# Performance work log

Hardware: AMD Instinct MI355X
Metric: run time of the kernel (lower is better)

## Reference

```python
import jax, jax.numpy as jnp
import numpy as np


def _mlp2(x, W1, b1, W2, b2):
    # two-layer MLP with ReLU hidden activation
    h = jax.nn.relu(jnp.einsum('...i,ij->...j', x, W1) + b1)
    return jnp.einsum('...i,ij->...j', h, W2) + b2


def setup_inputs() -> dict:
    key = jax.random.key(0)
    ks = jax.random.split(key, 8)
    B, N, D = 8, 256, 64
    positions = jax.random.normal(ks[0], (B, N, 3), dtype=jnp.float32)
    values = jax.random.normal(ks[1], (B, N, D), dtype=jnp.float32)
    # value_net: 2 -> D -> D ; score_net: D -> D -> 1 (He-style init)
    Wv1 = jax.random.normal(ks[2], (2, D), dtype=jnp.float32) * np.sqrt(2.0 / 2)
    bv1 = jnp.zeros((D,), dtype=jnp.float32)
    Wv2 = jax.random.normal(ks[3], (D, D), dtype=jnp.float32) * np.sqrt(2.0 / D)
    bv2 = jnp.zeros((D,), dtype=jnp.float32)
    Ws1 = jax.random.normal(ks[4], (D, D), dtype=jnp.float32) * np.sqrt(2.0 / D)
    bs1 = jnp.zeros((D,), dtype=jnp.float32)
    Ws2 = jax.random.normal(ks[5], (D, 1), dtype=jnp.float32) * np.sqrt(2.0 / D)
    bs2 = jnp.zeros((1,), dtype=jnp.float32)
    return dict(positions=positions, values=values, Wv1=Wv1, bv1=bv1, Wv2=Wv2,
                bv2=bv2, Ws1=Ws1, bs1=bs1, Ws2=Ws2, bs2=bs2)


def reference(positions, values, Wv1, bv1, Wv2, bv2, Ws1, bs1, Ws2, bs2):
    # rank-2 geometric algebra attention, reduce=True, merge_fun=join_fun='mean'
    B, N, _ = positions.shape
    r_i = positions[:, :, None, :]            # [B, N, 1, 3]
    r_j = positions[:, None, :, :]            # [B, 1, N, 3]
    # geometric product of two vectors -> scalar (dot) + bivector (wedge)
    dot = jnp.sum(r_i * r_j, axis=-1)         # [B, N, N] scalar part
    wedge = jnp.cross(r_i, r_j)               # [B, N, N, 3] bivector components
    biv_norm = jnp.sqrt(jnp.sum(wedge * wedge, axis=-1) + 1e-20)
    invariants = jnp.stack([dot, biv_norm], axis=-1)             # [B, N, N, 2]
    # merge_fun='mean' over the pair of node values
    merged = 0.5 * (values[:, :, None, :] + values[:, None, :, :])  # [B,N,N,D]
    invar_values = _mlp2(invariants, Wv1, bv1, Wv2, bv2)            # [B,N,N,D]
    # join_fun='mean' of value_net(invariants) and merged node values
    joined = 0.5 * (invar_values + merged)                          # [B,N,N,D]
    scores = _mlp2(joined, Ws1, bs1, Ws2, bs2)                      # [B,N,N,1]
    # reduce=True: softmax over all N*N product indices, output is [B, D]
    attn = jax.nn.softmax(scores.reshape(B, N * N), axis=-1).reshape(B, N, N, 1)
    output = jnp.sum(attn * joined, axis=(1, 2))                    # [B, D]
    return output
```

## Files before the change

kernel.cpp:

```cpp
#include <hip/hip_runtime.h>
#include <hip/hip_bf16.h>
#include <hip/hip_fp16.h>

#define NB 8
#define NN 256
#define DD 64

#define OFF_WCF   0
#define OFF_CSF   2048
#define OFF_CC    3584
#define OFF_MI    3648
#define OFF_RSI   5696
#define OFF_SHR   7744
#define OFF_P     138816
#define OFF_VF    269888

typedef __attribute__((ext_vector_type(4))) float f32x4;
typedef _Float16 f16x8 __attribute__((ext_vector_type(8)));

__global__ __launch_bounds__(256) void k_setup(
    const float* __restrict__ values, const float* __restrict__ Wv1,
    const float* __restrict__ bv1, const float* __restrict__ Wv2,
    const float* __restrict__ bv2, const float* __restrict__ Ws1,
    const float* __restrict__ bs1, float* __restrict__ ws)
{
    int idx = blockIdx.x * 256 + threadIdx.x;
    if (idx < 131072) {
        ((_Float16*)(ws + OFF_VF))[idx] = (_Float16)values[idx];
        int r = idx & 3, lane = (idx >> 2) & 63, nt = (idx >> 8) & 3, jtg = idx >> 10;
        int b = jtg >> 4, jt = jtg & 15;
        int j = jt * 16 + (lane >> 4) * 4 + r;
        int d = nt * 16 + (lane & 15);
        const float* v = values + (b * 256 + j) * 64;
        float s = 0.f;
#pragma unroll 8
        for (int k = 0; k < 64; k++) s = fmaf(v[k], Ws1[k * 64 + d], s);
        ws[OFF_P + idx] = 0.25f * s;
    } else if (idx < 135168) {
        int e = idx - 131072;
        int j = e & 7, ln = (e >> 3) & 63, nt = (e >> 9) & 3, ks = e >> 11;
        int k = ks * 32 + (ln >> 4) * 8 + j;
        int d = nt * 16 + (ln & 15);
        float s = 0.f;
#pragma unroll 8
        for (int m = 0; m < 64; m++) s = fmaf(Wv2[k * 64 + m], Ws1[m * 64 + d], s);
        ((_Float16*)(ws + OFF_WCF))[e] = (_Float16)(0.5f * s);
    } else if (idx < 138240) {
        int e = idx - 135168;
        int ln = e / 48;
        int rem = e - ln * 48;
        int coef = rem >> 4, kslot = rem & 15;
        int ks = kslot >> 3, j = kslot & 7;
        int k = ks * 32 + (ln >> 4) * 8 + j;
        float v = (coef == 0) ? Wv1[k] : (coef == 1) ? Wv1[64 + k] : bv1[k];
        ((_Float16*)(ws + OFF_CSF))[ln * 48 + coef * 16 + kslot] = (_Float16)v;
    } else if (idx < 138304) {
        int d = idx - 138240;
        float s = 0.f;
#pragma unroll 8
        for (int k = 0; k < 64; k++) s = fmaf(bv2[k], Ws1[k * 64 + d], s);
        ws[OFF_CC + d] = 0.5f * s + bs1[d];
    }
}

__global__ __launch_bounds__(256, 4) void k_main(
    const float* __restrict__ pos, const float* __restrict__ Wv1,
    const float* __restrict__ bv1, const float* __restrict__ Ws2,
    float* __restrict__ ws)
{
    __shared__ float2 ldsDB[256];
    __shared__ float  ldsS[256];
    __shared__ float  ldsCC[64];
    __shared__ float  ldsWs2[64];
    __shared__ float  ldsPos[3];
    __shared__ float  ldsRedM[4];
    __shared__ float  ldsRedS[4];
    __shared__ float  ldsP[4][64];

    int b = blockIdx.x >> 8;
    int i = blockIdx.x & 255;
    int t = threadIdx.x;
    int lane = t & 63, wv = t >> 6;
    int q = lane >> 4, col = lane & 15;

    f16x8 cfA[2], cfB[2], cfC[2];
    {
        const f16x8* cs = (const f16x8*)((const _Float16*)(ws + OFF_CSF) + lane * 48);
        cfA[0] = cs[0]; cfA[1] = cs[1];
        cfB[0] = cs[2]; cfB[1] = cs[3];
        cfC[0] = cs[4]; cfC[1] = cs[5];
    }
    f16x8 wcf[2][4];
    {
        const f16x8* p = (const f16x8*)(ws + OFF_WCF);
#pragma unroll
        for (int ks = 0; ks < 2; ks++)
#pragma unroll
            for (int nt = 0; nt < 4; nt++)
                wcf[ks][nt] = p[(ks * 4 + nt) * 64 + lane];
    }
    if (t < 3)  ldsPos[t] = pos[(b * 256 + i) * 3 + t];
    if (t >= 64 && t < 128) ldsCC[t - 64] = ws[OFF_CC + t - 64];
    if (t >= 128 && t < 192) ldsWs2[t - 128] = Ws2[t - 128];
    __syncthreads();

    {
        float px = pos[(b * 256 + t) * 3 + 0];
        float py = pos[(b * 256 + t) * 3 + 1];
        float pz = pos[(b * 256 + t) * 3 + 2];
        float ax = ldsPos[0], ay = ldsPos[1], az = ldsPos[2];
        float dot = ax * px + ay * py + az * pz;
        float cx = ay * pz - az * py;
        float cy = az * px - ax * pz;
        float cz = ax * py - ay * px;
        float biv = sqrtf(cx * cx + cy * cy + cz * cz + 1e-20f);
        ldsDB[t] = make_float2(dot, biv);
    }

    const float* Pb = ws + OFF_P + b * 16384;
    const _Float16* vfB = (const _Float16*)(ws + OFF_VF) + b * (NN * DD);

    float cu[4], w2r[4];
    {
        int jti = i >> 4, qq = (i >> 2) & 3, rr = i & 3;
#pragma unroll
        for (int nt = 0; nt < 4; nt++) {
            cu[nt] = ldsCC[nt * 16 + col] + Pb[(jti * 4 + nt) * 256 + qq * 64 + col * 4 + rr];
            w2r[nt] = ldsWs2[nt * 16 + col];
        }
    }

#pragma unroll
    for (int jt4 = 0; jt4 < 4; jt4++) {
        int jt = wv * 4 + jt4;
        const _Float16* vrow = vfB + (jt * 16 + col) * 64;
        f16x8 av0 = *(const f16x8*)(vrow + q * 8);
        f16x8 av1 = *(const f16x8*)(vrow + 32 + q * 8);
        f32x4 acc[4];
        const float* Pt = Pb + (jt * 4) * 256 + lane * 4;
#pragma unroll
        for (int nt = 0; nt < 4; nt++)
            acc[nt] = *(const f32x4*)(Pt + nt * 256);

        float2 db = ldsDB[jt * 16 + col];
        _Float16 dh = (_Float16)db.x, bh = (_Float16)db.y;
        f16x8 d8, b8;
#pragma unroll
        for (int p = 0; p < 8; p++) { d8[p] = dh; b8[p] = bh; }
        f16x8 af0, af1;
        {
            f16x8 h0 = d8 * cfA[0] + b8 * cfB[0] + cfC[0];
            f16x8 h1 = d8 * cfA[1] + b8 * cfB[1] + cfC[1];
            af0 = __builtin_elementwise_max(h0, (f16x8)(_Float16)0.f);
            af1 = __builtin_elementwise_max(h1, (f16x8)(_Float16)0.f);
        }
#pragma unroll
        for (int nt = 0; nt < 4; nt++) {
            acc[nt] = __builtin_amdgcn_mfma_f32_16x16x32_f16(av0, wcf[0][nt], acc[nt], 0, 0, 0);
            acc[nt] = __builtin_amdgcn_mfma_f32_16x16x32_f16(av1, wcf[1][nt], acc[nt], 0, 0, 0);
        }

        float tr[4] = {0.f, 0.f, 0.f, 0.f};
#pragma unroll
        for (int nt = 0; nt < 4; nt++) {
            f32x4 a2 = *(const f32x4*)(Pt + nt * 256);
            a2 = __builtin_amdgcn_mfma_f32_16x16x32_f16(af0, wcf[0][nt], a2, 0, 0, 0);
            a2 = __builtin_amdgcn_mfma_f32_16x16x32_f16(af1, wcf[1][nt], a2, 0, 0, 0);
#pragma unroll
            for (int r = 0; r < 4; r++) {
                float s = a2[r] + cu[nt];
                tr[r] = fmaf(fmaxf(s, 0.f), w2r[nt], tr[r]);
            }
        }
        (void)av0; (void)av1; (void)acc;
#pragma unroll
        for (int m = 1; m < 16; m <<= 1) {
#pragma unroll
            for (int r = 0; r < 4; r++) tr[r] += __shfl_xor(tr[r], m);
        }
        if (col == 0)
            *(float4*)&ldsS[jt * 16 + q * 4] = make_float4(tr[0], tr[1], tr[2], tr[3]);
    }

    float sv = ldsS[t];
    float wm = sv;
#pragma unroll
    for (int md = 1; md < 64; md <<= 1) wm = fmaxf(wm, __shfl_xor(wm, md));
    if (lane == 0) ldsRedM[wv] = wm;
    __syncthreads();
    float m_row = fmaxf(fmaxf(ldsRedM[0], ldsRedM[1]), fmaxf(ldsRedM[2], ldsRedM[3]));
    float wgt = __expf(sv - m_row);
    float rsp = wgt;
#pragma unroll
    for (int md = 1; md < 64; md <<= 1) rsp += __shfl_xor(rsp, md);
    ldsS[t] = wgt;
    if (lane == 0) ldsRedS[wv] = rsp;
    __syncthreads();
    float rowsum = ldsRedS[0] + ldsRedS[1] + ldsRedS[2] + ldsRedS[3];

    float A = Wv1[lane], B = Wv1[64 + lane], C = bv1[lane];
    float acc2 = 0.f;
#pragma unroll 8
    for (int jj = 0; jj < 64; jj++) {
        int j = wv * 64 + jj;
        float w = ldsS[j];
        float2 db = ldsDB[j];
        float h = fmaxf(fmaf(db.x, A, fmaf(db.y, B, C)), 0.f);
        acc2 = fmaf(w, h, acc2);
    }
    ldsP[wv][lane] = acc2;
    __syncthreads();
    if (t < 64)
        ws[OFF_SHR + (b * 256 + i) * 64 + t] = ldsP[0][t] + ldsP[1][t] + ldsP[2][t] + ldsP[3][t];
    if (t == 0) {
        ws[OFF_MI  + b * 256 + i] = m_row;
        ws[OFF_RSI + b * 256 + i] = rowsum;
    }
}

__global__ __launch_bounds__(256) void k_final(
    const float* __restrict__ values, const float* __restrict__ Wv2,
    const float* __restrict__ bv2, const float* __restrict__ ws,
    float* __restrict__ out)
{
    __shared__ float scl[256], zl[256], red[4], pS[4][64], pA[4][64], shv[64], a2v[64];
    int b = blockIdx.x, t = threadIdx.x, wv = t >> 6, lane = t & 63;

    float mi = ws[OFF_MI + b * 256 + t];
    float wm = mi;
#pragma unroll
    for (int md = 1; md < 64; md <<= 1) wm = fmaxf(wm, __shfl_xor(wm, md));
    if (lane == 0) red[wv] = wm;
    __syncthreads();
    float M = fmaxf(fmaxf(red[0], red[1]), fmaxf(red[2], red[3]));

    float rs = ws[OFF_RSI + b * 256 + t];
    float sc = __expf(mi - M);
    float zt = sc * rs;
    scl[t] = sc; zl[t] = zt;
    float zp = zt;
#pragma unroll
    for (int md = 1; md < 64; md <<= 1) zp += __shfl_xor(zp, md);
    __syncthreads();
    if (lane == 0) red[wv] = zp;
    __syncthreads();
    float Z = red[0] + red[1] + red[2] + red[3];

    float accS = 0.f, accA = 0.f;
    const float* shrB = ws + OFF_SHR + b * 256 * 64;
    const float* vB   = values + b * 256 * 64;
#pragma unroll 4
    for (int jj = 0; jj < 64; jj++) {
        int row = wv * 64 + jj;
        accS = fmaf(scl[row], shrB[row * 64 + lane], accS);
        accA = fmaf(zl[row],  vB[row * 64 + lane],  accA);
    }
    pS[wv][lane] = accS; pA[wv][lane] = accA;
    __syncthreads();
    if (t < 64) {
        shv[t] = pS[0][t] + pS[1][t] + pS[2][t] + pS[3][t];
        a2v[t] = pA[0][t] + pA[1][t] + pA[2][t] + pA[3][t];
    }
    __syncthreads();
    if (t < 64) {
        float t1 = 0.f;
#pragma unroll 8
        for (int k = 0; k < 64; k++) t1 = fmaf(shv[k], Wv2[k * 64 + t], t1);
        out[b * 64 + t] = 0.5f * (t1 + a2v[t]) / Z + 0.5f * bv2[t];
    }
}

extern "C" void kernel_launch(void* const* d_in, const int* in_sizes, int n_in,
                              void* d_out, int out_size, void* d_ws, size_t ws_size,
                              hipStream_t stream)
{
    const float* positions = (const float*)d_in[0];
    const float* values    = (const float*)d_in[1];
    const float* Wv1       = (const float*)d_in[2];
    const float* bv1       = (const float*)d_in[3];
    const float* Wv2       = (const float*)d_in[4];
    const float* bv2       = (const float*)d_in[5];
    const float* Ws1       = (const float*)d_in[6];
    const float* bs1       = (const float*)d_in[7];
    const float* Ws2       = (const float*)d_in[8];
    float* ws  = (float*)d_ws;
    float* out = (float*)d_out;

    k_setup<<<541, 256, 0, stream>>>(values, Wv1, bv1, Wv2, bv2, Ws1, bs1, ws);
    k_main<<<2048, 256, 0, stream>>>(positions, Wv1, bv1, Ws2, ws);
    k_final<<<NB, 256, 0, stream>>>(values, Wv2, bv2, ws, out);
}
```

Measured before the change: 107.7 us.

## Process two query rows per block, drop dead fp16 value path, widen final kernel

Each main-kernel block now handles two query rows i, reusing the loaded P tiles, weight fragments and position data across both rows, which halves the grid to 1024 blocks. The unused fp16 value conversion and the dead first MFMA chain, whose result was never consumed, are removed from setup and main. The final reduction kernel uses 1024 threads so each wave handles 16 rows instead of 64. This trades fewer blocks and more registers per thread (two cu sets, float4 LDS entries) for less redundant loading and compute.

```diff
diff --git a/kernel.cpp b/kernel.cpp
--- a/kernel.cpp
+++ b/kernel.cpp
@@ -13,7 +13,6 @@
 #define OFF_RSI   5696
 #define OFF_SHR   7744
 #define OFF_P     138816
-#define OFF_VF    269888
 
 typedef __attribute__((ext_vector_type(4))) float f32x4;
 typedef _Float16 f16x8 __attribute__((ext_vector_type(8)));
@@ -26,7 +25,6 @@
 {
     int idx = blockIdx.x * 256 + threadIdx.x;
     if (idx < 131072) {
-        ((_Float16*)(ws + OFF_VF))[idx] = (_Float16)values[idx];
         int r = idx & 3, lane = (idx >> 2) & 63, nt = (idx >> 8) & 3, jtg = idx >> 10;
         int b = jtg >> 4, jt = jtg & 15;
         int j = jt * 16 + (lane >> 4) * 4 + r;
@@ -68,18 +66,18 @@
     const float* __restrict__ bv1, const float* __restrict__ Ws2,
     float* __restrict__ ws)
 {
-    __shared__ float2 ldsDB[256];
-    __shared__ float  ldsS[256];
+    __shared__ float4 ldsDB[256];
+    __shared__ float2 ldsS[256];
     __shared__ float  ldsCC[64];
     __shared__ float  ldsWs2[64];
-    __shared__ float  ldsPos[3];
-    __shared__ float  ldsRedM[4];
-    __shared__ float  ldsRedS[4];
-    __shared__ float  ldsP[4][64];
-
-    int b = blockIdx.x >> 8;
-    int i = blockIdx.x & 255;
-    int t = threadIdx.x;
+    __shared__ float  ldsPos[6];
+    __shared__ float  ldsRedM[2][4];
+    __shared__ float  ldsRedS[2][4];
+    __shared__ float  ldsP[2][4][64];
+
+    int b  = blockIdx.x >> 7;
+    int i0 = (blockIdx.x & 127) * 2;
+    int t  = threadIdx.x;
     int lane = t & 63, wv = t >> 6;
     int q = lane >> 4, col = lane & 15;
 
@@ -99,7 +97,7 @@
             for (int nt = 0; nt < 4; nt++)
                 wcf[ks][nt] = p[(ks * 4 + nt) * 64 + lane];
     }
-    if (t < 3)  ldsPos[t] = pos[(b * 256 + i) * 3 + t];
+    if (t < 6)  ldsPos[t] = pos[(b * 256 + i0) * 3 + t];
     if (t >= 64 && t < 128) ldsCC[t - 64] = ws[OFF_CC + t - 64];
     if (t >= 128 && t < 192) ldsWs2[t - 128] = Ws2[t - 128];
     __syncthreads();
@@ -108,158 +106,184 @@
         float px = pos[(b * 256 + t) * 3 + 0];
         float py = pos[(b * 256 + t) * 3 + 1];
         float pz = pos[(b * 256 + t) * 3 + 2];
-        float ax = ldsPos[0], ay = ldsPos[1], az = ldsPos[2];
-        float dot = ax * px + ay * py + az * pz;
-        float cx = ay * pz - az * py;
-        float cy = az * px - ax * pz;
-        float cz = ax * py - ay * px;
-        float biv = sqrtf(cx * cx + cy * cy + cz * cz + 1e-20f);
-        ldsDB[t] = make_float2(dot, biv);
+        float4 r;
+        {
+            float ax = ldsPos[0], ay = ldsPos[1], az = ldsPos[2];
+            r.x = ax * px + ay * py + az * pz;
+            float cx = ay * pz - az * py, cy = az * px - ax * pz, cz = ax * py - ay * px;
+            r.y = sqrtf(cx * cx + cy * cy + cz * cz + 1e-20f);
+        }
+        {
+            float ax = ldsPos[3], ay = ldsPos[4], az = ldsPos[5];
+            r.z = ax * px + ay * py + az * pz;
+            float cx = ay * pz - az * py, cy = az * px - ax * pz, cz = ax * py - ay * px;
+            r.w = sqrtf(cx * cx + cy * cy + cz * cz + 1e-20f);
+        }
+        ldsDB[t] = r;
     }
 
     const float* Pb = ws + OFF_P + b * 16384;
-    const _Float16* vfB = (const _Float16*)(ws + OFF_VF) + b * (NN * DD);
-
-    float cu[4], w2r[4];
-    {
+
+    float cu[2][4], w2r[4];
+#pragma unroll
+    for (int ii = 0; ii < 2; ii++) {
+        int i = i0 + ii;
         int jti = i >> 4, qq = (i >> 2) & 3, rr = i & 3;
 #pragma unroll
-        for (int nt = 0; nt < 4; nt++) {
-            cu[nt] = ldsCC[nt * 16 + col] + Pb[(jti * 4 + nt) * 256 + qq * 64 + col * 4 + rr];
-            w2r[nt] = ldsWs2[nt * 16 + col];
-        }
-    }
+        for (int nt = 0; nt < 4; nt++)
+            cu[ii][nt] = ldsCC[nt * 16 + col] + Pb[(jti * 4 + nt) * 256 + qq * 64 + col * 4 + rr];
+    }
+#pragma unroll
+    for (int nt = 0; nt < 4; nt++) w2r[nt] = ldsWs2[nt * 16 + col];
 
 #pragma unroll
     for (int jt4 = 0; jt4 < 4; jt4++) {
         int jt = wv * 4 + jt4;
-        const _Float16* vrow = vfB + (jt * 16 + col) * 64;
-        f16x8 av0 = *(const f16x8*)(vrow + q * 8);
-        f16x8 av1 = *(const f16x8*)(vrow + 32 + q * 8);
-        f32x4 acc[4];
+        f32x4 ptile[4];
         const float* Pt = Pb + (jt * 4) * 256 + lane * 4;
 #pragma unroll
         for (int nt = 0; nt < 4; nt++)
-            acc[nt] = *(const f32x4*)(Pt + nt * 256);
-
-        float2 db = ldsDB[jt * 16 + col];
-        _Float16 dh = (_Float16)db.x, bh = (_Float16)db.y;
-        f16x8 d8, b8;
-#pragma unroll
-        for (int p = 0; p < 8; p++) { d8[p] = dh; b8[p] = bh; }
-        f16x8 af0, af1;
-        {
-            f16x8 h0 = d8 * cfA[0] + b8 * cfB[0] + cfC[0];
-            f16x8 h1 = d8 * cfA[1] + b8 * cfB[1] + cfC[1];
-            af0 = __builtin_elementwise_max(h0, (f16x8)(_Float16)0.f);
-            af1 = __builtin_elementwise_max(h1, (f16x8)(_Float16)0.f);
-        }
-#pragma unroll
-        for (int nt = 0; nt < 4; nt++) {
-            acc[nt] = __builtin_amdgcn_mfma_f32_16x16x32_f16(av0, wcf[0][nt], acc[nt], 0, 0, 0);
-            acc[nt] = __builtin_amdgcn_mfma_f32_16x16x32_f16(av1, wcf[1][nt], acc[nt], 0, 0, 0);
-        }
-
-        float tr[4] = {0.f, 0.f, 0.f, 0.f};
-#pragma unroll
-        for (int nt = 0; nt < 4; nt++) {
-            f32x4 a2 = *(const f32x4*)(Pt + nt * 256);
-            a2 = __builtin_amdgcn_mfma_f32_16x16x32_f16(af0, wcf[0][nt], a2, 0, 0, 0);
-            a2 = __builtin_amdgcn_mfma_f32_16x16x32_f16(af1, wcf[1][nt], a2, 0, 0, 0);
-#pragma unroll
-            for (int r = 0; r < 4; r++) {
-                float s = a2[r] + cu[nt];
-                tr[r] = fmaf(fmaxf(s, 0.f), w2r[nt], tr[r]);
+            ptile[nt] = *(const f32x4*)(Pt + nt * 256);
+
+        float4 db4 = ldsDB[jt * 16 + col];
+#pragma unroll
+        for (int ii = 0; ii < 2; ii++) {
+            _Float16 dh = (_Float16)(ii ? db4.z : db4.x);
+            _Float16 bh = (_Float16)(ii ? db4.w : db4.y);
+            f16x8 d8, b8;
+#pragma unroll
+            for (int p = 0; p < 8; p++) { d8[p] = dh; b8[p] = bh; }
+            f16x8 af0, af1;
+            {
+                f16x8 h0 = d8 * cfA[0] + b8 * cfB[0] + cfC[0];
+                f16x8 h1 = d8 * cfA[1] + b8 * cfB[1] + cfC[1];
+                af0 = __builtin_elementwise_max(h0, (f16x8)(_Float16)0.f);
+                af1 = __builtin_elementwise_max(h1, (f16x8)(_Float16)0.f);
+            }
+            float tr[4] = {0.f, 0.f, 0.f, 0.f};
+#pragma unroll
+            for (int nt = 0; nt < 4; nt++) {
+                f32x4 a2 = __builtin_amdgcn_mfma_f32_16x16x32_f16(af0, wcf[0][nt], ptile[nt], 0, 0, 0);
+                a2 = __builtin_amdgcn_mfma_f32_16x16x32_f16(af1, wcf[1][nt], a2, 0, 0, 0);
+#pragma unroll
+                for (int r = 0; r < 4; r++) {
+                    float s = a2[r] + cu[ii][nt];
+                    tr[r] = fmaf(fmaxf(s, 0.f), w2r[nt], tr[r]);
+                }
+            }
+#pragma unroll
+            for (int m = 1; m < 16; m <<= 1) {
+#pragma unroll
+                for (int r = 0; r < 4; r++) tr[r] += __shfl_xor(tr[r], m);
+            }
+            if (col == 0) {
+#pragma unroll
+                for (int r = 0; r < 4; r++)
+                    ldsS[jt * 16 + q * 4 + r][ii] = tr[r];
             }
         }
-        (void)av0; (void)av1; (void)acc;
-#pragma unroll
-        for (int m = 1; m < 16; m <<= 1) {
-#pragma unroll
-            for (int r = 0; r < 4; r++) tr[r] += __shfl_xor(tr[r], m);
-        }
-        if (col == 0)
-            *(float4*)&ldsS[jt * 16 + q * 4] = make_float4(tr[0], tr[1], tr[2], tr[3]);
-    }
-
-    float sv = ldsS[t];
-    float wm = sv;
-#pragma unroll
-    for (int md = 1; md < 64; md <<= 1) wm = fmaxf(wm, __shfl_xor(wm, md));
-    if (lane == 0) ldsRedM[wv] = wm;
-    __syncthreads();
-    float m_row = fmaxf(fmaxf(ldsRedM[0], ldsRedM[1]), fmaxf(ldsRedM[2], ldsRedM[3]));
-    float wgt = __expf(sv - m_row);
-    float rsp = wgt;
-#pragma unroll
-    for (int md = 1; md < 64; md <<= 1) rsp += __shfl_xor(rsp, md);
-    ldsS[t] = wgt;
-    if (lane == 0) ldsRedS[wv] = rsp;
-    __syncthreads();
-    float rowsum = ldsRedS[0] + ldsRedS[1] + ldsRedS[2] + ldsRedS[3];
+    }
+
+    float2 sv = ldsS[t];
+    float wm0 = sv.x, wm1 = sv.y;
+#pragma unroll
+    for (int md = 1; md < 64; md <<= 1) {
+        wm0 = fmaxf(wm0, __shfl_xor(wm0, md));
+        wm1 = fmaxf(wm1, __shfl_xor(wm1, md));
+    }
+    if (lane == 0) { ldsRedM[0][wv] = wm0; ldsRedM[1][wv] = wm1; }
+    __syncthreads();
+    float m0 = fmaxf(fmaxf(ldsRedM[0][0], ldsRedM[0][1]), fmaxf(ldsRedM[0][2], ldsRedM[0][3]));
+    float m1 = fmaxf(fmaxf(ldsRedM[1][0], ldsRedM[1][1]), fmaxf(ldsRedM[1][2], ldsRedM[1][3]));
+    float w0 = __expf(sv.x - m0), w1 = __expf(sv.y - m1);
+    float rs0 = w0, rs1 = w1;
+#pragma unroll
+    for (int md = 1; md < 64; md <<= 1) {
+        rs0 += __shfl_xor(rs0, md);
+        rs1 += __shfl_xor(rs1, md);
+    }
+    ldsS[t] = make_float2(w0, w1);
+    if (lane == 0) { ldsRedS[0][wv] = rs0; ldsRedS[1][wv] = rs1; }
+    __syncthreads();
+    float rowsum0 = ldsRedS[0][0] + ldsRedS[0][1] + ldsRedS[0][2] + ldsRedS[0][3];
+    float rowsum1 = ldsRedS[1][0] + ldsRedS[1][1] + ldsRedS[1][2] + ldsRedS[1][3];
 
     float A = Wv1[lane], B = Wv1[64 + lane], C = bv1[lane];
-    float acc2 = 0.f;
+    float acc0 = 0.f, acc1 = 0.f;
 #pragma unroll 8
     for (int jj = 0; jj < 64; jj++) {
         int j = wv * 64 + jj;
-        float w = ldsS[j];
-        float2 db = ldsDB[j];
-        float h = fmaxf(fmaf(db.x, A, fmaf(db.y, B, C)), 0.f);
-        acc2 = fmaf(w, h, acc2);
-    }
-    ldsP[wv][lane] = acc2;
-    __syncthreads();
-    if (t < 64)
-        ws[OFF_SHR + (b * 256 + i) * 64 + t] = ldsP[0][t] + ldsP[1][t] + ldsP[2][t] + ldsP[3][t];
+        float2 wj = ldsS[j];
+        float4 db = ldsDB[j];
+        float h0 = fmaxf(fmaf(db.x, A, fmaf(db.y, B, C)), 0.f);
+        float h1 = fmaxf(fmaf(db.z, A, fmaf(db.w, B, C)), 0.f);
+        acc0 = fmaf(wj.x, h0, acc0);
+        acc1 = fmaf(wj.y, h1, acc1);
+    }
+    ldsP[0][wv][lane] = acc0;
+    ldsP[1][wv][lane] = acc1;
+    __syncthreads();
+    if (t < 128) {
+        int ii = t >> 6, k = t & 63;
+        ws[OFF_SHR + (b * 256 + i0 + ii) * 64 + k] =
+            ldsP[ii][0][k] + ldsP[ii][1][k] + ldsP[ii][2][k] + ldsP[ii][3][k];
+    }
     if (t == 0) {
-        ws[OFF_MI  + b * 256 + i] = m_row;
-        ws[OFF_RSI + b * 256 + i] = rowsum;
+        ws[OFF_MI  + b * 256 + i0]     = m0;
+        ws[OFF_MI  + b * 256 + i0 + 1] = m1;
+        ws[OFF_RSI + b * 256 + i0]     = rowsum0;
+        ws[OFF_RSI + b * 256 + i0 + 1] = rowsum1;
     }
 }
 
-__global__ __launch_bounds__(256) void k_final(
+__global__ __launch_bounds__(1024) void k_final(
     const float* __restrict__ values, const float* __restrict__ Wv2,
     const float* __restrict__ bv2, const float* __restrict__ ws,
     float* __restrict__ out)
 {
-    __shared__ float scl[256], zl[256], red[4], pS[4][64], pA[4][64], shv[64], a2v[64];
+    __shared__ float scl[256], zl[256], redM[4], redZ[4];
+    __shared__ float pS[16][64], pA[16][64], shv[64], a2v[64];
     int b = blockIdx.x, t = threadIdx.x, wv = t >> 6, lane = t & 63;
 
-    float mi = ws[OFF_MI + b * 256 + t];
-    float wm = mi;
-#pragma unroll
-    for (int md = 1; md < 64; md <<= 1) wm = fmaxf(wm, __shfl_xor(wm, md));
-    if (lane == 0) red[wv] = wm;
-    __syncthreads();
-    float M = fmaxf(fmaxf(red[0], red[1]), fmaxf(red[2], red[3]));
-
-    float rs = ws[OFF_RSI + b * 256 + t];
-    float sc = __expf(mi - M);
-    float zt = sc * rs;
-    scl[t] = sc; zl[t] = zt;
-    float zp = zt;
-#pragma unroll
-    for (int md = 1; md < 64; md <<= 1) zp += __shfl_xor(zp, md);
-    __syncthreads();
-    if (lane == 0) red[wv] = zp;
-    __syncthreads();
-    float Z = red[0] + red[1] + red[2] + red[3];
+    float mi = 0.f;
+    if (t < 256) {
+        mi = ws[OFF_MI + b * 256 + t];
+        float wm = mi;
+#pragma unroll
+        for (int md = 1; md < 64; md <<= 1) wm = fmaxf(wm, __shfl_xor(wm, md));
+        if (lane == 0) redM[wv] = wm;
+    }
+    __syncthreads();
+    if (t < 256) {
+        float M = fmaxf(fmaxf(redM[0], redM[1]), fmaxf(redM[2], redM[3]));
+        float rs = ws[OFF_RSI + b * 256 + t];
+        float sc = __expf(mi - M);
+        float zt = sc * rs;
+        scl[t] = sc; zl[t] = zt;
+        float zp = zt;
+#pragma unroll
+        for (int md = 1; md < 64; md <<= 1) zp += __shfl_xor(zp, md);
+        if (lane == 0) redZ[wv] = zp;
+    }
+    __syncthreads();
+    float Z = redZ[0] + redZ[1] + redZ[2] + redZ[3];
 
     float accS = 0.f, accA = 0.f;
     const float* shrB = ws + OFF_SHR + b * 256 * 64;
     const float* vB   = values + b * 256 * 64;
-#pragma unroll 4
-    for (int jj = 0; jj < 64; jj++) {
-        int row = wv * 64 + jj;
+#pragma unroll
+    for (int jj = 0; jj < 16; jj++) {
+        int row = wv * 16 + jj;
         accS = fmaf(scl[row], shrB[row * 64 + lane], accS);
         accA = fmaf(zl[row],  vB[row * 64 + lane],  accA);
     }
     pS[wv][lane] = accS; pA[wv][lane] = accA;
     __syncthreads();
     if (t < 64) {
-        shv[t] = pS[0][t] + pS[1][t] + pS[2][t] + pS[3][t];
-        a2v[t] = pA[0][t] + pA[1][t] + pA[2][t] + pA[3][t];
+        float s1 = 0.f, s2 = 0.f;
+#pragma unroll
+        for (int w = 0; w < 16; w++) { s1 += pS[w][t]; s2 += pA[w][t]; }
+        shv[t] = s1; a2v[t] = s2;
     }
     __syncthreads();
     if (t < 64) {
@@ -287,6 +311,6 @@
     float* out = (float*)d_out;
 
     k_setup<<<541, 256, 0, stream>>>(values, Wv1, bv1, Wv2, bv2, Ws1, bs1, ws);
-    k_main<<<2048, 256, 0, stream>>>(positions, Wv1, bv1, Ws2, ws);
-    k_final<<<NB, 256, 0, stream>>>(values, Wv2, bv2, ws, out);
+    k_main<<<1024, 256, 0, stream>>>(positions, Wv1, bv1, Ws2, ws);
+    k_final<<<NB, 1024, 0, stream>>>(values, Wv2, bv2, ws, out);
 }
```

Measured after the change: 101.0 us (median of 2 runs). 1.07x faster.
